# Optimization experiments

Measured on AMD Instinct MI355X. Metric: run time of the kernel, lower is better.

## Reference

```python
import jax, jax.numpy as jnp
import numpy as np

B, CIN, COUT, H, W = 16, 64, 64, 128, 128
KH, KW = 3, 3
PAD, STRIDE = 1, 1


def setup_inputs() -> dict:
    key = jax.random.key(0)
    k1, k2 = jax.random.split(key)
    x = jax.random.normal(k1, (B, CIN, H, W), dtype=jnp.float32)
    scale = (1.0 / (CIN * KH * KW)) ** 0.5
    weight = jax.random.normal(k2, (COUT, CIN, KH, KW), dtype=jnp.float32) * scale
    bias = jnp.zeros((COUT,), dtype=jnp.float32)
    return {"x": x, "weight": weight, "bias": bias}


def reference(x, weight, bias):
    # Faithful translation of FFTConv2d.forward (including its einsum semantics:
    # 'bchw,oihw->bohw' sums over c and i independently, as in the torch source).
    b, c, h, w = x.shape
    kh, kw = weight.shape[2], weight.shape[3]
    pad_h = h + kh - 1  # 130
    pad_w = w + kw - 1  # 130
    x_padded = jnp.pad(x, ((0, 0), (0, 0), (0, pad_h - h), (0, pad_w - w)))
    w_padded = jnp.pad(weight, ((0, 0), (0, 0), (0, pad_h - kh), (0, pad_w - kw)))
    X_fft = jnp.fft.rfft2(x_padded)                  # [B,C,pad_h,pad_w//2+1]
    W_fft = jnp.fft.rfft2(w_padded, s=(pad_h, pad_w))  # [O,I,pad_h,pad_w//2+1]
    Y_fft = jnp.einsum('bchw,oihw->bohw', X_fft, W_fft)
    y = jnp.fft.irfft2(Y_fft, s=(pad_h, pad_w))      # [B,O,pad_h,pad_w]
    # torch: y[:, :, padding:-padding or None:stride, padding:-padding or None:stride]
    y = y[:, :, PAD:-PAD:STRIDE, PAD:-PAD:STRIDE]    # [B,O,H,W] for PAD=1,STRIDE=1
    y = y + bias[None, :, None, None]
    return y
```

## Files before the change

kernel.cpp:

```cpp
#include <hip/hip_runtime.h>

typedef float f32x4 __attribute__((ext_vector_type(4)));

#define NB 16
#define NC 64
#define NH 128
#define NW 128
#define STRIPE 8
#define LROWS (STRIPE + 2)
#define LCOLS 136

__global__ __launch_bounds__(512) void fused_conv_kernel(
    const float* __restrict__ x, const float* __restrict__ wgt,
    const float* __restrict__ bias, float* __restrict__ out) {
  __shared__ float xs[LROWS][LCOLS];
  __shared__ float red[64][9][3];
  __shared__ float wl[64][12];

  const int t   = threadIdx.x;
  const int bid = blockIdx.x;
  const int b   = bid >> 4;
  const int R0  = (bid & 15) * STRIPE;

  if (t < 320) {
    const int row = t >> 5;
    const int g   = t & 31;
    const int ir  = R0 - 1 + row;
    f32x4 a0 = {0,0,0,0}, a1 = {0,0,0,0}, a2 = {0,0,0,0}, a3 = {0,0,0,0};
    if (ir >= 0 && ir < NH) {
      const float* xp = x + (b * NC * NH + ir) * NW + g * 4;
      #pragma unroll 4
      for (int c = 0; c < NC; c += 4) {
        a0 += *(const f32x4*)(xp + (c + 0) * (NH * NW));
        a1 += *(const f32x4*)(xp + (c + 1) * (NH * NW));
        a2 += *(const f32x4*)(xp + (c + 2) * (NH * NW));
        a3 += *(const f32x4*)(xp + (c + 3) * (NH * NW));
      }
    }
    *(f32x4*)&xs[row][4 + g * 4] = (a0 + a1) + (a2 + a3);
    if (t < 2 * LROWS) xs[t >> 1][(t & 1) ? 132 : 3] = 0.f;
  } else {
    const int idx   = t - 320;
    const int o     = idx / 3;
    const int third = idx - o * 3;
    const int c0    = (third * NC) / 3;
    const int c1    = ((third + 1) * NC) / 3;
    const float* wp = wgt + o * (NC * 9);
    float part[9] = {0.f, 0.f, 0.f, 0.f, 0.f, 0.f, 0.f, 0.f, 0.f};
    for (int i = c0; i < c1; ++i) {
      #pragma unroll
      for (int k = 0; k < 9; ++k) part[k] += wp[i * 9 + k];
    }
    #pragma unroll
    for (int k = 0; k < 9; ++k) red[o][k][third] = part[k];
  }
  __syncthreads();

  for (int s = t; s < 576; s += 512) {
    int o  = s / 9;
    int t9 = s - o * 9;
    wl[o][8 - t9] = red[o][t9][0] + red[o][t9][1] + red[o][t9][2];
  }
  if (t < 64) wl[t][9] = bias[t];
  __syncthreads();

  {
    const int ohalf = t >> 8;
    const int r5    = t & 255;
    const int ro    = r5 >> 5;
    const int g     = r5 & 31;
    const int q0    = g * 4;
    float X0[6], X1[6], X2[6];
    #pragma unroll
    for (int m = 0; m < 6; ++m) {
      X0[m] = xs[ro][q0 + 3 + m];
      X1[m] = xs[ro + 1][q0 + 3 + m];
      X2[m] = xs[ro + 2][q0 + 3 + m];
    }
    float* op = out + ((b * 64 + ohalf * 32) * NH + R0 + ro) * NW + q0;
    for (int oi = 0; oi < 32; ++oi) {
      const int o = ohalf * 32 + oi;
      f32x4 wa = *(const f32x4*)&wl[o][0];
      f32x4 wb = *(const f32x4*)&wl[o][4];
      f32x4 wc = *(const f32x4*)&wl[o][8];
      f32x4 y;
      #pragma unroll
      for (int jj = 0; jj < 4; ++jj) {
        float acc = wc[1];
        acc += wa[0] * X0[jj] + wa[1] * X0[jj + 1] + wa[2] * X0[jj + 2];
        acc += wa[3] * X1[jj] + wb[0] * X1[jj + 1] + wb[1] * X1[jj + 2];
        acc += wb[2] * X2[jj] + wb[3] * X2[jj + 1] + wc[0] * X2[jj + 2];
        y[jj] = acc;
      }
      *(f32x4*)(op + oi * (NH * NW)) = y;
    }
  }
}

extern "C" void kernel_launch(void* const* d_in, const int* in_sizes, int n_in,
                              void* d_out, int out_size, void* d_ws, size_t ws_size,
                              hipStream_t stream) {
  const float* x    = (const float*)d_in[0];
  const float* wgt  = (const float*)d_in[1];
  const float* bias = (const float*)d_in[2];
  float* out = (float*)d_out;
  (void)in_sizes; (void)n_in; (void)out_size; (void)d_ws; (void)ws_size;

  fused_conv_kernel<<<dim3(NB * (NH / STRIPE)), dim3(512), 0, stream>>>(x, wgt, bias, out);
}
```

Measured before the change: 123.7 us.

## Split each row stripe into column halves with 256-thread blocks and single sync

```diff
diff --git a/kernel.cpp b/kernel.cpp
--- a/kernel.cpp
+++ b/kernel.cpp
@@ -7,79 +7,78 @@
 #define NH 128
 #define NW 128
 #define STRIPE 8
-#define LROWS (STRIPE + 2)
-#define LCOLS 136
+#define LROWS 10
+#define LCOLS 72
 
-__global__ __launch_bounds__(512) void fused_conv_kernel(
+__global__ __launch_bounds__(256, 4) void fused_conv_kernel(
     const float* __restrict__ x, const float* __restrict__ wgt,
     const float* __restrict__ bias, float* __restrict__ out) {
   __shared__ float xs[LROWS][LCOLS];
-  __shared__ float red[64][9][3];
   __shared__ float wl[64][12];
 
   const int t   = threadIdx.x;
   const int bid = blockIdx.x;
-  const int b   = bid >> 4;
-  const int R0  = (bid & 15) * STRIPE;
+  const int b   = bid >> 5;
+  const int r5  = bid & 31;
+  const int R0  = (r5 >> 1) * STRIPE;
+  const int h   = r5 & 1;
+  const int ch0 = h * 64;
+  const int w0  = ch0 - 4;
 
-  if (t < 320) {
-    const int row = t >> 5;
-    const int g   = t & 31;
+  if (t < 180) {
+    const int row = t / 18;
+    const int g   = t - row * 18;
     const int ir  = R0 - 1 + row;
-    f32x4 a0 = {0,0,0,0}, a1 = {0,0,0,0}, a2 = {0,0,0,0}, a3 = {0,0,0,0};
-    if (ir >= 0 && ir < NH) {
-      const float* xp = x + (b * NC * NH + ir) * NW + g * 4;
-      #pragma unroll 4
-      for (int c = 0; c < NC; c += 4) {
-        a0 += *(const f32x4*)(xp + (c + 0) * (NH * NW));
-        a1 += *(const f32x4*)(xp + (c + 1) * (NH * NW));
-        a2 += *(const f32x4*)(xp + (c + 2) * (NH * NW));
-        a3 += *(const f32x4*)(xp + (c + 3) * (NH * NW));
+    const int q0  = w0 + g * 4;
+    f32x4 s0 = {0,0,0,0}, s1 = {0,0,0,0}, s2 = {0,0,0,0}, s3 = {0,0,0,0};
+    f32x4 s4 = {0,0,0,0}, s5 = {0,0,0,0}, s6 = {0,0,0,0}, s7 = {0,0,0,0};
+    if (ir >= 0 && ir < NH && q0 >= 0 && q0 <= NW - 4) {
+      const float* xp = x + (b * NC * NH + ir) * NW + q0;
+      #pragma unroll
+      for (int c = 0; c < NC; c += 8) {
+        s0 += *(const f32x4*)(xp + (c + 0) * (NH * NW));
+        s1 += *(const f32x4*)(xp + (c + 1) * (NH * NW));
+        s2 += *(const f32x4*)(xp + (c + 2) * (NH * NW));
+        s3 += *(const f32x4*)(xp + (c + 3) * (NH * NW));
+        s4 += *(const f32x4*)(xp + (c + 4) * (NH * NW));
+        s5 += *(const f32x4*)(xp + (c + 5) * (NH * NW));
+        s6 += *(const f32x4*)(xp + (c + 6) * (NH * NW));
+        s7 += *(const f32x4*)(xp + (c + 7) * (NH * NW));
       }
     }
-    *(f32x4*)&xs[row][4 + g * 4] = (a0 + a1) + (a2 + a3);
-    if (t < 2 * LROWS) xs[t >> 1][(t & 1) ? 132 : 3] = 0.f;
+    *(f32x4*)&xs[row][g * 4] = ((s0 + s1) + (s2 + s3)) + ((s4 + s5) + (s6 + s7));
   } else {
-    const int idx   = t - 320;
-    const int o     = idx / 3;
-    const int third = idx - o * 3;
-    const int c0    = (third * NC) / 3;
-    const int c1    = ((third + 1) * NC) / 3;
-    const float* wp = wgt + o * (NC * 9);
-    float part[9] = {0.f, 0.f, 0.f, 0.f, 0.f, 0.f, 0.f, 0.f, 0.f};
-    for (int i = c0; i < c1; ++i) {
-      #pragma unroll
-      for (int k = 0; k < 9; ++k) part[k] += wp[i * 9 + k];
+    for (int s = t - 180; s < 640; s += 76) {
+      if (s < 576) {
+        const int o  = s / 9;
+        const int t9 = s - o * 9;
+        const float* wp = wgt + o * (NC * 9) + t9;
+        float acc = 0.f;
+        #pragma unroll 8
+        for (int i = 0; i < NC; ++i) acc += wp[i * 9];
+        wl[o][8 - t9] = acc;
+      } else {
+        wl[s - 576][9] = bias[s - 576];
+      }
     }
-    #pragma unroll
-    for (int k = 0; k < 9; ++k) red[o][k][third] = part[k];
   }
   __syncthreads();
 
-  for (int s = t; s < 576; s += 512) {
-    int o  = s / 9;
-    int t9 = s - o * 9;
-    wl[o][8 - t9] = red[o][t9][0] + red[o][t9][1] + red[o][t9][2];
-  }
-  if (t < 64) wl[t][9] = bias[t];
-  __syncthreads();
-
   {
-    const int ohalf = t >> 8;
-    const int r5    = t & 255;
-    const int ro    = r5 >> 5;
-    const int g     = r5 & 31;
-    const int q0    = g * 4;
+    const int oh = t >> 7;
+    const int sp = t & 127;
+    const int ro = sp >> 4;
+    const int g  = sp & 15;
     float X0[6], X1[6], X2[6];
     #pragma unroll
     for (int m = 0; m < 6; ++m) {
-      X0[m] = xs[ro][q0 + 3 + m];
-      X1[m] = xs[ro + 1][q0 + 3 + m];
-      X2[m] = xs[ro + 2][q0 + 3 + m];
+      X0[m] = xs[ro][4 * g + 3 + m];
+      X1[m] = xs[ro + 1][4 * g + 3 + m];
+      X2[m] = xs[ro + 2][4 * g + 3 + m];
     }
-    float* op = out + ((b * 64 + ohalf * 32) * NH + R0 + ro) * NW + q0;
+    float* op = out + ((b * 64 + oh * 32) * NH + R0 + ro) * NW + ch0 + 4 * g;
     for (int oi = 0; oi < 32; ++oi) {
-      const int o = ohalf * 32 + oi;
+      const int o = oh * 32 + oi;
       f32x4 wa = *(const f32x4*)&wl[o][0];
       f32x4 wb = *(const f32x4*)&wl[o][4];
       f32x4 wc = *(const f32x4*)&wl[o][8];
@@ -106,5 +105,5 @@
   float* out = (float*)d_out;
   (void)in_sizes; (void)n_in; (void)out_size; (void)d_ws; (void)ws_size;
 
-  fused_conv_kernel<<<dim3(NB * (NH / STRIPE)), dim3(512), 0, stream>>>(x, wgt, bias, out);
+  fused_conv_kernel<<<dim3(NB * 16 * 2), dim3(256), 0, stream>>>(x, wgt, bias, out);
 }
```

Result: slower. 143.3 us (+15.9%).
